# Kernel tuning notes

Measured on AMD Instinct MI355X. Metric: run time of the kernel, lower is better.

## Reference

```python
import jax, jax.numpy as jnp
import numpy as np

N = 50000
E = 500000
NODE_F = 128
POS_F = 3
COORD_F = 64
EDGE_IN = 2 * NODE_F + 1  # 257


def _linear_params(key, fan_in, fan_out):
    k1, k2 = jax.random.split(key)
    bound = 1.0 / np.sqrt(fan_in)
    W = jax.random.uniform(k1, (fan_in, fan_out), jnp.float32, -bound, bound)
    b = jax.random.uniform(k2, (fan_out,), jnp.float32, -bound, bound)
    return W, b


def setup_inputs() -> dict:
    key = jax.random.key(0)
    ks = jax.random.split(key, 8)
    x = jax.random.normal(ks[0], (N, NODE_F + POS_F), jnp.float32)
    edge_index = jax.random.randint(ks[1], (2, E), 0, N, jnp.int64)
    W_e1, b_e1 = _linear_params(ks[2], EDGE_IN, 2 * EDGE_IN)
    W_e2, b_e2 = _linear_params(ks[3], 2 * EDGE_IN, COORD_F)
    W_c1, b_c1 = _linear_params(ks[4], COORD_F, 4 * COORD_F)
    W_c2, b_c2 = _linear_params(ks[5], 4 * COORD_F, 1)
    W_n1, b_n1 = _linear_params(ks[6], NODE_F + COORD_F, 2 * NODE_F)
    W_n2, b_n2 = _linear_params(ks[7], 2 * NODE_F, NODE_F)
    return {"x": x, "edge_index": edge_index,
            "W_e1": W_e1, "b_e1": b_e1, "W_e2": W_e2, "b_e2": b_e2,
            "W_c1": W_c1, "b_c1": b_c1, "W_c2": W_c2, "b_c2": b_c2,
            "W_n1": W_n1, "b_n1": b_n1, "W_n2": W_n2, "b_n2": b_n2}


def reference(x, edge_index, W_e1, b_e1, W_e2, b_e2, W_c1, b_c1, W_c2, b_c2,
              W_n1, b_n1, W_n2, b_n2):
    node = x[:, :-POS_F]            # (N, 128)
    coords = x[:, -POS_F:]          # (N, 3)
    src = edge_index[0]             # j (source)
    dst = edge_index[1]             # i (target)

    rel_coords = coords[src] - coords[dst]                          # (E, 3)
    rel_dist = jnp.sqrt(jnp.sum(rel_coords ** 2, -1, keepdims=True))  # (E, 1)

    # message: edge_mlp(cat[x_i, x_j, edge_attr])
    e_in = jnp.concatenate([node[dst], node[src], rel_dist], axis=-1)  # (E, 257)
    h = jax.nn.silu(e_in @ W_e1 + b_e1)
    m_ij = jax.nn.silu(h @ W_e2 + b_e2)                             # (E, 64)
    coord_w = jax.nn.silu(m_ij @ W_c1 + b_c1) @ W_c2 + b_c2         # (E, 1)

    # scatter-sum aggregation to target nodes
    m_i = jax.ops.segment_sum(m_ij, dst, num_segments=N)            # (N, 64)
    w_i = jax.ops.segment_sum(coord_w, dst, num_segments=N)         # (N, 1)
    r_i = jax.ops.segment_sum(rel_coords, dst, num_segments=N)      # (N, 3)

    coords_out = coords + w_i * r_i
    n_in = jnp.concatenate([node, m_i], axis=-1)                    # (N, 192)
    hidden = jax.nn.silu(n_in @ W_n1 + b_n1) @ W_n2 + b_n2 + node   # (N, 128)
    return jnp.concatenate([hidden, coords_out], axis=-1)           # (N, 131)
```

## Files before the change

### kernel.cpp

```cpp
#include <hip/hip_runtime.h>
#include <hip/hip_bf16.h>
#include <hip/hip_fp16.h>

#define NN 50000
#define NE 500000
#define DCAP 48

using bf16x8 = __attribute__((ext_vector_type(8))) short;
using f16x8  = __attribute__((ext_vector_type(8))) _Float16;
using f32x4  = __attribute__((ext_vector_type(4))) float;
using f32x2  = __attribute__((ext_vector_type(2))) float;

__device__ __forceinline__ float b2f(unsigned short s) {
  union { unsigned u; float f; } v; v.u = ((unsigned)s) << 16; return v.f;
}
__device__ __forceinline__ unsigned short f2b(float f) {
  __hip_bfloat16 h = __float2bfloat16(f);
  return *reinterpret_cast<unsigned short*>(&h);
}
__device__ __forceinline__ unsigned short f2h(float f) {
  __half h = __float2half(f);
  return *reinterpret_cast<unsigned short*>(&h);
}
__device__ __forceinline__ float hu2f(unsigned short s) {
  __half h; *reinterpret_cast<unsigned short*>(&h) = s; return __half2float(h);
}
__device__ __forceinline__ unsigned pack2(float a, float b) {
  __hip_bfloat162 h = __float22bfloat162_rn(make_float2(a, b));
  return *reinterpret_cast<unsigned*>(&h);
}
__device__ __forceinline__ unsigned pack2h(float a, float b) {
  __half2 h = __float22half2_rn(make_float2(a, b));
  return *reinterpret_cast<unsigned*>(&h);
}
__device__ __forceinline__ __half2 h2u(unsigned u) {
  union { unsigned v; __half2 h; } x; x.v = u; return x.h;
}
__device__ __forceinline__ unsigned u2h(__half2 h) {
  union { __half2 h; unsigned v; } x; x.h = h; return x.v;
}
__device__ __forceinline__ float silu_f(float x) {
  return x * __builtin_amdgcn_rcpf(1.f + __expf(-x));
}
__device__ __forceinline__ __half2 silu2(__half2 z) {
  const __half2 one = __float2half2_rn(1.f);
  __half2 e = h2exp(__hneg2(z));
  return __hmul2(z, h2rcp(__hadd2(e, one)));
}

#define WPREP 269344
#define B0 (WPREP + NN * 17)
#define B1 (B0 + NN)
#define B2 (B1 + 1)
#define PREP_TOTAL (B2 + NE)
__global__ void prep_all(const float* __restrict__ we1,
                         const float* __restrict__ be1,
                         const float* __restrict__ we2,
                         const float* __restrict__ be2,
                         const float* __restrict__ wc1,
                         const float* __restrict__ wn1,
                         const float* __restrict__ wn2,
                         const float* __restrict__ x,
                         unsigned short* __restrict__ A1p,
                         unsigned short* __restrict__ A2p,
                         unsigned short* __restrict__ AdB,
                         unsigned short* __restrict__ W2p,
                         unsigned short* __restrict__ Wc1p,
                         unsigned short* __restrict__ Wn1p,
                         unsigned short* __restrict__ Wn2p,
                         float* __restrict__ be1p,
                         unsigned short* __restrict__ node_p,
                         float* __restrict__ coords_p,
                         int* __restrict__ cnt,
                         int* __restrict__ total,
                         int* __restrict__ esrc) {
  int i = blockIdx.x * 256 + threadIdx.x;
  if (i < 67584) {
    int n = i / 128, k = i % 128;
    A1p[i] = (n < 514) ? f2b(we1[k * 514 + n]) : (unsigned short)0;
  } else if (i < 135168) {
    int j = i - 67584; int n = j / 128, k = j % 128;
    A2p[j] = (n < 514) ? f2b(we1[(128 + k) * 514 + n]) : (unsigned short)0;
  } else if (i < 135696) {
    int j = i - 135168;
    AdB[j] = (j < 514) ? f2h(we1[256 * 514 + j]) : (unsigned short)0;
  } else if (i < 170512) {
    int j = i - 135696; int n = j / 544, lk = j % 544;
    unsigned short v = 0;
    if (lk < 514) v = f2h(we2[lk * 64 + n]);
    else if (lk == 514) v = f2h(be2[n]);
    W2p[j] = v;
  } else if (i < 186896) {
    int j = i - 170512; int n = j / 64, k = j % 64;
    Wc1p[j] = f2b(wc1[k * 256 + n]);
  } else if (i < 236048) {
    int j = i - 186896; int n = j / 192, k = j % 192;
    Wn1p[j] = f2b(wn1[k * 256 + n]);
  } else if (i < 268816) {
    int j = i - 236048; int n = j / 256, k = j % 256;
    Wn2p[j] = f2b(wn2[k * 128 + n]);
  } else if (i < WPREP) {
    int j = i - 268816;
    be1p[j] = (j < 514) ? be1[j] : 0.f;
  } else if (i < B0) {
    int j = i - WPREP;
    if (j < NN * 16) {
      int g = j >> 4, c = j & 15;
      const float* s = x + g * 131 + c * 8;
      unsigned short* d = node_p + g * 128 + c * 8;
#pragma unroll
      for (int q = 0; q < 8; q++) d[q] = f2b(s[q]);
    } else {
      int g = j - NN * 16;
      float4 c;
      c.x = x[g * 131 + 128];
      c.y = x[g * 131 + 129];
      c.z = x[g * 131 + 130];
      c.w = 0.f;
      *(float4*)(coords_p + g * 4) = c;
    }
  } else if (i < B1) {
    cnt[i - B0] = 0;
  } else if (i < B2) {
    total[0] = 0;
  } else if (i < PREP_TOTAL) {
    esrc[i - B2] = -1;
  }
}

__global__ void build_adj(const int* __restrict__ eidx,
                          int* __restrict__ cnt, int* __restrict__ adj) {
  int e = blockIdx.x * 256 + threadIdx.x;
  if (e < NE) {
    int d = eidx[NE + e];
    d = min(max(d, 0), NN - 1);
    int slot = atomicAdd(&cnt[d], 1);
    if (slot < DCAP) adj[d * DCAP + slot] = e;
  }
}

__global__ void assign_off(const int* __restrict__ cnt,
                           int* __restrict__ off,
                           int* __restrict__ total) {
  int g = blockIdx.x * 256 + threadIdx.x;
  int lane = threadIdx.x & 63;
  int deg = (g < NN) ? min(cnt[g], DCAP) : 0;
  int incl = deg;
#pragma unroll
  for (int d = 1; d < 64; d <<= 1) {
    int v = __shfl_up(incl, d, 64);
    if (lane >= d) incl += v;
  }
  int wsum = __shfl(incl, 63, 64);
  int base = 0;
  if (lane == 63) base = atomicAdd(total, wsum);
  base = __shfl(base, 63, 64);
  if (g < NN) off[g] = base + incl - deg;
}

__global__ void compact_adj(const int* __restrict__ cnt,
                            const int* __restrict__ off,
                            const int* __restrict__ adj,
                            const int* __restrict__ eidx,
                            const float* __restrict__ coords_p,
                            int* __restrict__ esrc,
                            int* __restrict__ edst,
                            float* __restrict__ scoord) {
  int t = blockIdx.x * 256 + threadIdx.x;
  if (t >= NN * DCAP) return;
  int g = t / DCAP, k = t % DCAP;
  int deg = min(cnt[g], DCAP);
  if (k >= deg) return;
  int e = adj[t];
  int s = eidx[e];
  s = min(max(s, 0), NN - 1);
  int o = off[g] + k;
  esrc[o] = s;
  edst[o] = g;
  float4 cs = *(const float4*)(coords_p + s * 4);
  float4 cd = *(const float4*)(coords_p + g * 4);
  float rx = cs.x - cd.x, ry = cs.y - cd.y, rz = cs.z - cd.z;
  float4 sc;
  sc.x = rx; sc.y = ry; sc.z = rz;
  sc.w = sqrtf(rx * rx + ry * ry + rz * rz);
  *(float4*)(scoord + (size_t)o * 4) = sc;
}

__launch_bounds__(256, 2)
__global__ void pgemm_kernel(const unsigned short* __restrict__ node_p,
                             const unsigned short* __restrict__ A1p,
                             const unsigned short* __restrict__ A2p,
                             const float* __restrict__ be1p,
                             unsigned short* __restrict__ P1,
                             unsigned char* __restrict__ P2) {
  __shared__ unsigned short sNode[64][136];
  int tid = threadIdx.x, blk = blockIdx.x;
  int lane = tid & 63, wv = tid >> 6, l16 = lane & 15, quad = lane >> 4;
#pragma unroll
  for (int it = 0; it < 4; it++) {
    int t = tid + it * 256;
    int row = t >> 4, ch = t & 15;
    int g = blk * 64 + row;
    if (g >= NN) g = 0;
    *(bf16x8*)(&sNode[row][ch * 8]) = *(const bf16x8*)(node_p + g * 128 + ch * 8);
  }
  __syncthreads();
#pragma unroll 1
  for (int t = 0; t < 9; t++) {
    int T = wv + 4 * t;
    if (T >= 33) break;
    f32x4 a1[4], a2[4];
#pragma unroll
    for (int s = 0; s < 4; s++) {
      a1[s] = (f32x4){0.f, 0.f, 0.f, 0.f};
      a2[s] = (f32x4){0.f, 0.f, 0.f, 0.f};
    }
    for (int kb = 0; kb < 4; kb++) {
      bf16x8 b1 = *(const bf16x8*)(A1p + (T * 16 + l16) * 128 + kb * 32 + quad * 8);
      bf16x8 b2 = *(const bf16x8*)(A2p + (T * 16 + l16) * 128 + kb * 32 + quad * 8);
#pragma unroll
      for (int s = 0; s < 4; s++) {
        bf16x8 a = *(const bf16x8*)(&sNode[s * 16 + l16][kb * 32 + quad * 8]);
        a1[s] = __builtin_amdgcn_mfma_f32_16x16x32_bf16(b1, a, a1[s], 0, 0, 0);
        a2[s] = __builtin_amdgcn_mfma_f32_16x16x32_bf16(b2, a, a2[s], 0, 0, 0);
      }
    }
    int nb = T * 16 + quad * 4;
    float4 b4 = *(const float4*)(be1p + nb);
    bool v0 = nb + 0 < 514, v1 = nb + 1 < 514, v2 = nb + 2 < 514, v3 = nb + 3 < 514;
#pragma unroll
    for (int s = 0; s < 4; s++) {
      int g = blk * 64 + s * 16 + l16;
      if (g < NN) {
        float p0 = v0 ? a1[s][0] + b4.x : 0.f;
        float p1v = v1 ? a1[s][1] + b4.y : 0.f;
        float p2v = v2 ? a1[s][2] + b4.z : 0.f;
        float p3 = v3 ? a1[s][3] + b4.w : 0.f;
        *(uint2*)(P1 + g * 528 + nb) = make_uint2(pack2h(p0, p1v), pack2h(p2v, p3));
        float q0 = v0 ? a2[s][0] : 0.f;
        float q1 = v1 ? a2[s][1] : 0.f;
        float q2 = v2 ? a2[s][2] : 0.f;
        float q3 = v3 ? a2[s][3] : 0.f;
        int w8 = __builtin_amdgcn_cvt_pk_fp8_f32(q0, q1, 0, false);
        w8 = __builtin_amdgcn_cvt_pk_fp8_f32(q2, q3, w8, true);
        *(unsigned*)(P2 + g * 528 + nb) = (unsigned)w8;
      }
    }
  }
}

__launch_bounds__(256, 3)
__global__ void edge_kernel(const unsigned short* __restrict__ P1,
                            const unsigned char* __restrict__ P2,
                            const unsigned short* __restrict__ AdB,
                            const int* __restrict__ esrcA,
                            const int* __restrict__ edstA,
                            const float* __restrict__ scoord,
                            const unsigned short* __restrict__ W2p,
                            const unsigned short* __restrict__ Wc1p,
                            const float* __restrict__ bc1,
                            const float* __restrict__ bc2,
                            const float* __restrict__ wc2,
                            unsigned short* __restrict__ medge,
                            float* __restrict__ coordw) {
  __shared__ unsigned short sHc[48][168];
  __shared__ unsigned short sM[48][72];
  __shared__ int sDst[48];
  __shared__ int sSrc[48];
  __shared__ int sE[48];
  __shared__ float sDistF[48];
  __shared__ float sCwPart[4][48];
  int tid = threadIdx.x, blk = blockIdx.x;
  int lane = tid & 63, wv = tid >> 6, l16 = lane & 15, quad = lane >> 4;

  unsigned tailP1 = 0u, tailP2 = 0u;
  if (tid < 48) {
    int r = blk * 48 + tid;
    int s = (r < NE) ? esrcA[r] : -1;
    sE[tid] = s;
    int ss = (s < 0) ? 0 : s;
    int d = 0;
    float dist = 0.f;
    if (s >= 0) {
      d = edstA[r];
      d = min(max(d, 0), NN - 1);
      dist = scoord[(size_t)r * 4 + 3];
    }
    sDst[tid] = d;
    sSrc[tid] = ss;
    sDistF[tid] = dist;
    tailP1 = *(const unsigned*)(P1 + d * 528 + 512);
    tailP2 = *(const unsigned*)(P2 + ss * 528 + 512);
  }
  __syncthreads();

  int cg = tid & 15, er = tid >> 4;
  const unsigned short* p1b[3];
  const unsigned char* p2b[3];
  __half2 d2[3];
#pragma unroll
  for (int it = 0; it < 3; it++) {
    int edge = er + it * 16;
    p1b[it] = P1 + sDst[edge] * 528 + cg * 8;
    p2b[it] = P2 + sSrc[edge] * 528 + cg * 8;
    d2[it] = __float2half2_rn(sDistF[edge]);
  }
  const unsigned short* adB = AdB + cg * 8;
  const unsigned short* w2b = W2p + (wv * 16 + l16) * 544 + quad * 8;

  uint2 u2r[4][3];
#pragma unroll
  for (int ch = 0; ch < 4; ch++)
#pragma unroll
    for (int it = 0; it < 3; it++)
      u2r[ch][it] = *(const uint2*)(p2b[it] + ch * 128);

  f32x4 macc[3];
#pragma unroll
  for (int s = 0; s < 3; s++) macc[s] = (f32x4){0.f, 0.f, 0.f, 0.f};

#pragma unroll
  for (int ch = 0; ch < 4; ch++) {
    uint4 uva = *(const uint4*)(adB + ch * 128);
    __half2 va0 = h2u(uva.x), va1 = h2u(uva.y), va2 = h2u(uva.z), va3 = h2u(uva.w);
#pragma unroll
    for (int it = 0; it < 3; it++) {
      int edge = er + it * 16;
      uint4 u1 = *(const uint4*)(p1b[it] + ch * 128);
      uint2 u2 = u2r[ch][it];
      f32x2 c0 = __builtin_amdgcn_cvt_pk_f32_fp8((int)u2.x, false);
      f32x2 c1 = __builtin_amdgcn_cvt_pk_f32_fp8((int)u2.x, true);
      f32x2 c2 = __builtin_amdgcn_cvt_pk_f32_fp8((int)u2.y, false);
      f32x2 c3 = __builtin_amdgcn_cvt_pk_f32_fp8((int)u2.y, true);
      __half2 q0 = h2u(pack2h(c0.x, c0.y));
      __half2 q1 = h2u(pack2h(c1.x, c1.y));
      __half2 q2 = h2u(pack2h(c2.x, c2.y));
      __half2 q3 = h2u(pack2h(c3.x, c3.y));
      __half2 z0 = __hfma2(va0, d2[it], __hadd2(h2u(u1.x), q0));
      __half2 z1 = __hfma2(va1, d2[it], __hadd2(h2u(u1.y), q1));
      __half2 z2 = __hfma2(va2, d2[it], __hadd2(h2u(u1.z), q2));
      __half2 z3 = __hfma2(va3, d2[it], __hadd2(h2u(u1.w), q3));
      *(uint4*)(&sHc[edge][cg * 8]) = make_uint4(
          u2h(silu2(z0)), u2h(silu2(z1)), u2h(silu2(z2)), u2h(silu2(z3)));
    }
    if (ch == 3 && tid < 48) {
      float dist = sDistF[tid];
      __half2 hp1 = h2u(tailP1);
      f32x2 t2 = __builtin_amdgcn_cvt_pk_f32_fp8((int)tailP2, false);
      float h512 = silu_f(__low2float(hp1) + t2.x + dist * hu2f(AdB[512]));
      float h513 = silu_f(__high2float(hp1) + t2.y + dist * hu2f(AdB[513]));
      *(uint4*)(&sHc[tid][128]) = make_uint4(pack2h(h512, h513), pack2h(1.0f, 0.f), 0u, 0u);
      *(uint4*)(&sHc[tid][136]) = make_uint4(0u, 0u, 0u, 0u);
      *(uint4*)(&sHc[tid][144]) = make_uint4(0u, 0u, 0u, 0u);
      *(uint4*)(&sHc[tid][152]) = make_uint4(0u, 0u, 0u, 0u);
    }
    __syncthreads();
    const int nkb = (ch == 3) ? 5 : 4;
#pragma unroll
    for (int kb = 0; kb < nkb; kb++) {
      f16x8 b = *(const f16x8*)(w2b + ch * 128 + kb * 32);
#pragma unroll
      for (int s = 0; s < 3; s++) {
        f16x8 a = *(const f16x8*)(&sHc[s * 16 + l16][kb * 32 + quad * 8]);
        macc[s] = __builtin_amdgcn_mfma_f32_16x16x32_f16(b, a, macc[s], 0, 0, 0);
      }
    }
    __syncthreads();
  }

  {
    int nb = wv * 16 + quad * 4;
#pragma unroll
    for (int s = 0; s < 3; s++) {
      unsigned lo = pack2(silu_f(macc[s][0]), silu_f(macc[s][1]));
      unsigned hi = pack2(silu_f(macc[s][2]), silu_f(macc[s][3]));
      *(uint2*)(&sM[s * 16 + l16][nb]) = make_uint2(lo, hi);
    }
  }
  __syncthreads();

  {
    float cw[3] = {0.f, 0.f, 0.f};
#pragma unroll
    for (int jt = 0; jt < 4; jt++) {
      int T = wv * 4 + jt;
      f32x4 cacc[3];
#pragma unroll
      for (int s = 0; s < 3; s++) cacc[s] = (f32x4){0.f, 0.f, 0.f, 0.f};
#pragma unroll
      for (int kb = 0; kb < 2; kb++) {
        bf16x8 b = *(const bf16x8*)(Wc1p + (T * 16 + l16) * 64 + kb * 32 + quad * 8);
#pragma unroll
        for (int s = 0; s < 3; s++) {
          bf16x8 a = *(const bf16x8*)(&sM[s * 16 + l16][kb * 32 + quad * 8]);
          cacc[s] = __builtin_amdgcn_mfma_f32_16x16x32_bf16(b, a, cacc[s], 0, 0, 0);
        }
      }
      int nb = T * 16 + quad * 4;
      float4 b4 = *(const float4*)(bc1 + nb);
      float4 w4 = *(const float4*)(wc2 + nb);
#pragma unroll
      for (int s = 0; s < 3; s++) {
        cw[s] += silu_f(cacc[s][0] + b4.x) * w4.x;
        cw[s] += silu_f(cacc[s][1] + b4.y) * w4.y;
        cw[s] += silu_f(cacc[s][2] + b4.z) * w4.z;
        cw[s] += silu_f(cacc[s][3] + b4.w) * w4.w;
      }
    }
#pragma unroll
    for (int s = 0; s < 3; s++) {
      cw[s] += __shfl_xor(cw[s], 16, 64);
      cw[s] += __shfl_xor(cw[s], 32, 64);
    }
    if (quad == 0) {
#pragma unroll
      for (int s = 0; s < 3; s++) sCwPart[wv][s * 16 + l16] = cw[s];
    }
  }
  __syncthreads();
#pragma unroll
  for (int it = 0; it < 2; it++) {
    int idx = it * 256 + tid;
    if (idx < 384) {
      int row = idx >> 3, ch8 = idx & 7;
      int r = blk * 48 + row;
      if (r < NE && sE[row] >= 0)
        *(bf16x8*)(medge + (size_t)r * 64 + ch8 * 8) = *(const bf16x8*)(&sM[row][ch8 * 8]);
    }
  }
  if (tid < 48) {
    int r = blk * 48 + tid;
    if (r < NE && sE[tid] >= 0) {
      float v = sCwPart[0][tid] + sCwPart[1][tid] + sCwPart[2][tid] + sCwPart[3][tid]
                + bc2[0];
      coordw[r] = v;
    }
  }
}

__launch_bounds__(256, 2)
__global__ void node_mlp_kernel(const unsigned short* __restrict__ node_p,
                                const float* __restrict__ x,
                                const float* __restrict__ coords_p,
                                const unsigned short* __restrict__ medge,
                                const float* __restrict__ coordw,
                                const float* __restrict__ scoord,
                                const int* __restrict__ cnt,
                                const int* __restrict__ off,
                                const unsigned short* __restrict__ Wn1p,
                                const unsigned short* __restrict__ Wn2p,
                                const float* __restrict__ bn1,
                                const float* __restrict__ bn2,
                                float* __restrict__ out) {
  __shared__ unsigned short sNin[64][200];
  __shared__ unsigned short sHid[64][264];
  __shared__ float sWr[64][4];
  int tid = threadIdx.x, blk = blockIdx.x;
  int lane = tid & 63, wv = tid >> 6, l16 = lane & 15, quad = lane >> 4;

#pragma unroll
  for (int it = 0; it < 4; it++) {
    int t = tid + it * 256;
    int row = t >> 4, ch = t & 15;
    int g = blk * 64 + row;
    if (g >= NN) g = 0;
    *(bf16x8*)(&sNin[row][ch * 8]) = *(const bf16x8*)(node_p + g * 128 + ch * 8);
  }
  {
    int row = tid >> 2, c = tid & 3;
    int g = blk * 64 + row;
    int gg = (g < NN) ? g : 0;
    int deg = min(cnt[gg], DCAP);
    int o = off[gg];
    float acc[16];
#pragma unroll
    for (int i = 0; i < 16; i++) acc[i] = 0.f;
    float sc = 0.f;
    for (int k = 0; k < deg; k++) {
      int r = o + k;
      const unsigned short* mrow = medge + (size_t)r * 64 + c * 16;
      bf16x8 a0 = *(const bf16x8*)(mrow);
      bf16x8 a1 = *(const bf16x8*)(mrow + 8);
#pragma unroll
      for (int i = 0; i < 8; i++) acc[i] += b2f((unsigned short)a0[i]);
#pragma unroll
      for (int i = 0; i < 8; i++) acc[8 + i] += b2f((unsigned short)a1[i]);
      sc += (c == 3) ? coordw[r] : scoord[(size_t)r * 4 + c];
    }
    unsigned u[8];
#pragma unroll
    for (int i = 0; i < 8; i++) u[i] = pack2(acc[2 * i], acc[2 * i + 1]);
    *(uint4*)(&sNin[row][128 + c * 16]) = make_uint4(u[0], u[1], u[2], u[3]);
    *(uint4*)(&sNin[row][128 + c * 16 + 8]) = make_uint4(u[4], u[5], u[6], u[7]);
    sWr[row][c] = sc;
  }
  __syncthreads();
  {
    f32x4 acc[4][4];
#pragma unroll
    for (int j = 0; j < 4; j++)
#pragma unroll
      for (int s = 0; s < 4; s++) acc[j][s] = (f32x4){0.f, 0.f, 0.f, 0.f};
    for (int kb = 0; kb < 6; kb++) {
      bf16x8 afr[4], bfr[4];
#pragma unroll
      for (int s = 0; s < 4; s++)
        afr[s] = *(const bf16x8*)(&sNin[s * 16 + l16][kb * 32 + quad * 8]);
#pragma unroll
      for (int j = 0; j < 4; j++)
        bfr[j] = *(const bf16x8*)(Wn1p + ((wv * 4 + j) * 16 + l16) * 192 + kb * 32 + quad * 8);
#pragma unroll
      for (int j = 0; j < 4; j++)
#pragma unroll
        for (int s = 0; s < 4; s++)
          acc[j][s] = __builtin_amdgcn_mfma_f32_16x16x32_bf16(bfr[j], afr[s], acc[j][s], 0, 0, 0);
    }
#pragma unroll
    for (int j = 0; j < 4; j++) {
      int nb = (wv * 4 + j) * 16 + quad * 4;
      float4 b4 = *(const float4*)(bn1 + nb);
#pragma unroll
      for (int s = 0; s < 4; s++) {
        unsigned lo = pack2(silu_f(acc[j][s][0] + b4.x), silu_f(acc[j][s][1] + b4.y));
        unsigned hi = pack2(silu_f(acc[j][s][2] + b4.z), silu_f(acc[j][s][3] + b4.w));
        *(uint2*)(&sHid[s * 16 + l16][nb]) = make_uint2(lo, hi);
      }
    }
  }
  __syncthreads();
  {
    f32x4 acc[2][4];
#pragma unroll
    for (int j = 0; j < 2; j++)
#pragma unroll
      for (int s = 0; s < 4; s++) acc[j][s] = (f32x4){0.f, 0.f, 0.f, 0.f};
    for (int kb = 0; kb < 8; kb++) {
      bf16x8 afr[4], bfr[2];
#pragma unroll
      for (int s = 0; s < 4; s++)
        afr[s] = *(const bf16x8*)(&sHid[s * 16 + l16][kb * 32 + quad * 8]);
#pragma unroll
      for (int j = 0; j < 2; j++)
        bfr[j] = *(const bf16x8*)(Wn2p + ((wv * 2 + j) * 16 + l16) * 256 + kb * 32 + quad * 8);
#pragma unroll
      for (int j = 0; j < 2; j++)
#pragma unroll
        for (int s = 0; s < 4; s++)
          acc[j][s] = __builtin_amdgcn_mfma_f32_16x16x32_bf16(bfr[j], afr[s], acc[j][s], 0, 0, 0);
    }
#pragma unroll
    for (int j = 0; j < 2; j++) {
      int nb = (wv * 2 + j) * 16 + quad * 4;
      float4 b4 = *(const float4*)(bn2 + nb);
#pragma unroll
      for (int s = 0; s < 4; s++) {
        int g = blk * 64 + s * 16 + l16;
        if (g < NN) {
          int base = g * 131 + nb;
          out[base + 0] = acc[j][s][0] + b4.x + x[base + 0];
          out[base + 1] = acc[j][s][1] + b4.y + x[base + 1];
          out[base + 2] = acc[j][s][2] + b4.z + x[base + 2];
          out[base + 3] = acc[j][s][3] + b4.w + x[base + 3];
        }
      }
    }
  }
  if (tid < 64) {
    int g = blk * 64 + tid;
    if (g < NN) {
      float w = sWr[tid][3];
      out[g * 131 + 128] = coords_p[g * 4 + 0] + w * sWr[tid][0];
      out[g * 131 + 129] = coords_p[g * 4 + 1] + w * sWr[tid][1];
      out[g * 131 + 130] = coords_p[g * 4 + 2] + w * sWr[tid][2];
    }
  }
}

extern "C" void kernel_launch(void* const* d_in, const int* in_sizes, int n_in,
                              void* d_out, int out_size, void* d_ws, size_t ws_size,
                              hipStream_t stream) {
  const float* x   = (const float*)d_in[0];
  const int* eidx  = (const int*)d_in[1];
  const float* we1 = (const float*)d_in[2];
  const float* be1 = (const float*)d_in[3];
  const float* we2 = (const float*)d_in[4];
  const float* be2 = (const float*)d_in[5];
  const float* wc1 = (const float*)d_in[6];
  const float* bc1 = (const float*)d_in[7];
  const float* wc2 = (const float*)d_in[8];
  const float* bc2 = (const float*)d_in[9];
  const float* wn1 = (const float*)d_in[10];
  const float* bn1 = (const float*)d_in[11];
  const float* wn2 = (const float*)d_in[12];
  const float* bn2 = (const float*)d_in[13];

  char* ws = (char*)d_ws;
  unsigned short* A1p    = (unsigned short*)(ws + 0);
  unsigned short* A2p    = (unsigned short*)(ws + 135168);
  unsigned short* AdB    = (unsigned short*)(ws + 270336);
  unsigned short* W2p    = (unsigned short*)(ws + 271392);
  unsigned short* Wc1p   = (unsigned short*)(ws + 341024);
  unsigned short* Wn1p   = (unsigned short*)(ws + 373792);
  unsigned short* Wn2p   = (unsigned short*)(ws + 472096);
  float* be1p            = (float*)(ws + 537632);
  unsigned short* node_p = (unsigned short*)(ws + 539744);
  float* coords_p        = (float*)(ws + 13339744);
  unsigned short* medge  = (unsigned short*)(ws + 14139744);
  float* coordw          = (float*)(ws + 78139744);
  int* cnt               = (int*)(ws + 80139744);
  int* adj               = (int*)(ws + 80339744);
  unsigned short* P1     = (unsigned short*)(ws + 103539744);
  unsigned char* P2      = (unsigned char*)(ws + 156339744);
  int* off               = (int*)(ws + 209139744);
  int* edst              = (int*)(ws + 209339748);
  int* esrc              = (int*)(ws + 211339748);
  int* total             = (int*)(ws + 213339748);
  float* scoord          = (float*)(ws + 213339760);

  prep_all<<<(PREP_TOTAL + 255) / 256, 256, 0, stream>>>(
      we1, be1, we2, be2, wc1, wn1, wn2, x,
      A1p, A2p, AdB, W2p, Wc1p, Wn1p, Wn2p, be1p, node_p, coords_p,
      cnt, total, esrc);
  pgemm_kernel<<<(NN + 63) / 64, 256, 0, stream>>>(node_p, A1p, A2p, be1p, P1, P2);
  build_adj<<<(NE + 255) / 256, 256, 0, stream>>>(eidx, cnt, adj);
  assign_off<<<(NN + 255) / 256, 256, 0, stream>>>(cnt, off, total);
  compact_adj<<<(NN * DCAP + 255) / 256, 256, 0, stream>>>(cnt, off, adj, eidx,
                                                           coords_p, esrc, edst,
                                                           scoord);
  edge_kernel<<<(NE + 47) / 48, 256, 0, stream>>>(P1, P2, AdB, esrc, edst, scoord,
                                                  W2p, Wc1p, bc1, bc2, wc2,
                                                  medge, coordw);
  node_mlp_kernel<<<(NN + 63) / 64, 256, 0, stream>>>(node_p, x, coords_p, medge,
                                                      coordw, scoord, cnt, off,
                                                      Wn1p, Wn2p, bn1, bn2,
                                                      (float*)d_out);
}
```

Measured before the change: 425.2 us.

## Fuse segment-sum into edge kernel via run-length atomic adds

Replaces the per-edge materialisation of bf16 messages and coordinate weights with atomic accumulation into per-node fp32 buffers directly from the edge kernel. Edges are sorted by destination, so consecutive edges with the same target are pre-summed before each atomic. The node MLP then reads pre-aggregated sums instead of walking adjacency lists. This removes a large intermediate write/read round trip, at the cost of atomic contention, zero-initialisation of the buffers, and non-deterministic summation order.

```diff
diff --git a/kernel.cpp b/kernel.cpp
--- a/kernel.cpp
+++ b/kernel.cpp
@@ -52,7 +52,9 @@
 #define B0 (WPREP + NN * 17)
 #define B1 (B0 + NN)
 #define B2 (B1 + 1)
-#define PREP_TOTAL (B2 + NE)
+#define B3 (B2 + NE)
+#define B4 (B3 + NN * 16)
+#define PREP_TOTAL (B4 + NN)
 __global__ void prep_all(const float* __restrict__ we1,
                          const float* __restrict__ be1,
                          const float* __restrict__ we2,
@@ -73,7 +75,9 @@
                          float* __restrict__ coords_p,
                          int* __restrict__ cnt,
                          int* __restrict__ total,
-                         int* __restrict__ esrc) {
+                         int* __restrict__ esrc,
+                         float* __restrict__ m_i,
+                         float* __restrict__ wr) {
   int i = blockIdx.x * 256 + threadIdx.x;
   if (i < 67584) {
     int n = i / 128, k = i % 128;
@@ -123,8 +127,14 @@
     cnt[i - B0] = 0;
   } else if (i < B2) {
     total[0] = 0;
+  } else if (i < B3) {
+    esrc[i - B2] = -1;
+  } else if (i < B4) {
+    int j = i - B3;
+    *(float4*)(m_i + (size_t)j * 4) = make_float4(0.f, 0.f, 0.f, 0.f);
   } else if (i < PREP_TOTAL) {
-    esrc[i - B2] = -1;
+    int j = i - B4;
+    *(float4*)(wr + j * 4) = make_float4(0.f, 0.f, 0.f, 0.f);
   }
 }
 
@@ -261,8 +271,8 @@
                             const float* __restrict__ bc1,
                             const float* __restrict__ bc2,
                             const float* __restrict__ wc2,
-                            unsigned short* __restrict__ medge,
-                            float* __restrict__ coordw) {
+                            float* __restrict__ m_i,
+                            float* __restrict__ wr) {
   __shared__ unsigned short sHc[48][168];
   __shared__ unsigned short sM[48][72];
   __shared__ int sDst[48];
@@ -418,22 +428,37 @@
     }
   }
   __syncthreads();
-#pragma unroll
-  for (int it = 0; it < 2; it++) {
-    int idx = it * 256 + tid;
-    if (idx < 384) {
-      int row = idx >> 3, ch8 = idx & 7;
-      int r = blk * 48 + row;
-      if (r < NE && sE[row] >= 0)
-        *(bf16x8*)(medge + (size_t)r * 64 + ch8 * 8) = *(const bf16x8*)(&sM[row][ch8 * 8]);
-    }
-  }
-  if (tid < 48) {
-    int r = blk * 48 + tid;
-    if (r < NE && sE[tid] >= 0) {
-      float v = sCwPart[0][tid] + sCwPart[1][tid] + sCwPart[2][tid] + sCwPart[3][tid]
-                + bc2[0];
-      coordw[r] = v;
+
+  {
+    int c = tid & 63, q = tid >> 6;
+    float acc = 0.f; int cur = -1;
+#pragma unroll
+    for (int e0 = 0; e0 < 12; e0++) {
+      int e = q * 12 + e0;
+      if (sE[e] < 0) continue;
+      int d = sDst[e];
+      float v = b2f(sM[e][c]);
+      if (d != cur) {
+        if (cur >= 0) atomicAdd(&m_i[(size_t)cur * 64 + c], acc);
+        cur = d; acc = v;
+      } else {
+        acc += v;
+      }
+    }
+    if (cur >= 0) atomicAdd(&m_i[(size_t)cur * 64 + c], acc);
+  }
+  if (tid < 192) {
+    int e = tid >> 2, comp = tid & 3;
+    if (sE[e] >= 0) {
+      int r = blk * 48 + e;
+      int d = sDst[e];
+      float val;
+      if (comp == 3)
+        val = sCwPart[0][e] + sCwPart[1][e] + sCwPart[2][e] + sCwPart[3][e]
+              + bc2[0];
+      else
+        val = scoord[(size_t)r * 4 + comp];
+      atomicAdd(&wr[d * 4 + comp], val);
     }
   }
 }
@@ -442,11 +467,8 @@
 __global__ void node_mlp_kernel(const unsigned short* __restrict__ node_p,
                                 const float* __restrict__ x,
                                 const float* __restrict__ coords_p,
-                                const unsigned short* __restrict__ medge,
-                                const float* __restrict__ coordw,
-                                const float* __restrict__ scoord,
-                                const int* __restrict__ cnt,
-                                const int* __restrict__ off,
+                                const float* __restrict__ m_i,
+                                const float* __restrict__ wr,
                                 const unsigned short* __restrict__ Wn1p,
                                 const unsigned short* __restrict__ Wn2p,
                                 const float* __restrict__ bn1,
@@ -470,29 +492,13 @@
     int row = tid >> 2, c = tid & 3;
     int g = blk * 64 + row;
     int gg = (g < NN) ? g : 0;
-    int deg = min(cnt[gg], DCAP);
-    int o = off[gg];
-    float acc[16];
-#pragma unroll
-    for (int i = 0; i < 16; i++) acc[i] = 0.f;
-    float sc = 0.f;
-    for (int k = 0; k < deg; k++) {
-      int r = o + k;
-      const unsigned short* mrow = medge + (size_t)r * 64 + c * 16;
-      bf16x8 a0 = *(const bf16x8*)(mrow);
-      bf16x8 a1 = *(const bf16x8*)(mrow + 8);
-#pragma unroll
-      for (int i = 0; i < 8; i++) acc[i] += b2f((unsigned short)a0[i]);
-#pragma unroll
-      for (int i = 0; i < 8; i++) acc[8 + i] += b2f((unsigned short)a1[i]);
-      sc += (c == 3) ? coordw[r] : scoord[(size_t)r * 4 + c];
-    }
-    unsigned u[8];
-#pragma unroll
-    for (int i = 0; i < 8; i++) u[i] = pack2(acc[2 * i], acc[2 * i + 1]);
-    *(uint4*)(&sNin[row][128 + c * 16]) = make_uint4(u[0], u[1], u[2], u[3]);
-    *(uint4*)(&sNin[row][128 + c * 16 + 8]) = make_uint4(u[4], u[5], u[6], u[7]);
-    sWr[row][c] = sc;
+    const float4* mi = (const float4*)(m_i + (size_t)gg * 64 + c * 16);
+    float4 v1 = mi[0], v2 = mi[1], v3 = mi[2], v4 = mi[3];
+    *(uint4*)(&sNin[row][128 + c * 16]) = make_uint4(
+        pack2(v1.x, v1.y), pack2(v1.z, v1.w), pack2(v2.x, v2.y), pack2(v2.z, v2.w));
+    *(uint4*)(&sNin[row][128 + c * 16 + 8]) = make_uint4(
+        pack2(v3.x, v3.y), pack2(v3.z, v3.w), pack2(v4.x, v4.y), pack2(v4.z, v4.w));
+    sWr[row][c] = wr[gg * 4 + c];
   }
   __syncthreads();
   {
@@ -605,8 +611,8 @@
   float* be1p            = (float*)(ws + 537632);
   unsigned short* node_p = (unsigned short*)(ws + 539744);
   float* coords_p        = (float*)(ws + 13339744);
-  unsigned short* medge  = (unsigned short*)(ws + 14139744);
-  float* coordw          = (float*)(ws + 78139744);
+  float* m_i             = (float*)(ws + 14139744);
+  float* wr              = (float*)(ws + 78139744);
   int* cnt               = (int*)(ws + 80139744);
   int* adj               = (int*)(ws + 80339744);
   unsigned short* P1     = (unsigned short*)(ws + 103539744);
@@ -620,7 +626,7 @@
   prep_all<<<(PREP_TOTAL + 255) / 256, 256, 0, stream>>>(
       we1, be1, we2, be2, wc1, wn1, wn2, x,
       A1p, A2p, AdB, W2p, Wc1p, Wn1p, Wn2p, be1p, node_p, coords_p,
-      cnt, total, esrc);
+      cnt, total, esrc, m_i, wr);
   pgemm_kernel<<<(NN + 63) / 64, 256, 0, stream>>>(node_p, A1p, A2p, be1p, P1, P2);
   build_adj<<<(NE + 255) / 256, 256, 0, stream>>>(eidx, cnt, adj);
   assign_off<<<(NN + 255) / 256, 256, 0, stream>>>(cnt, off, total);
@@ -629,9 +635,8 @@
                                                            scoord);
   edge_kernel<<<(NE + 47) / 48, 256, 0, stream>>>(P1, P2, AdB, esrc, edst, scoord,
                                                   W2p, Wc1p, bc1, bc2, wc2,
-                                                  medge, coordw);
-  node_mlp_kernel<<<(NN + 63) / 64, 256, 0, stream>>>(node_p, x, coords_p, medge,
-                                                      coordw, scoord, cnt, off,
+                                                  m_i, wr);
+  node_mlp_kernel<<<(NN + 63) / 64, 256, 0, stream>>>(node_p, x, coords_p, m_i, wr,
                                                       Wn1p, Wn2p, bn1, bn2,
                                                       (float*)d_out);
 }
```

Result: faster. 414.5 us (-2.5%).
